# Kernel optimization log

Hardware: AMD Instinct MI355X
Metric: run time of the kernel (lower is better)

The kernel has to match this reference:

```python
import jax, jax.numpy as jnp
import numpy as np

KS = 3                 # kernel_size
DILATIONS = (1, 2, 3)  # dilation list
NUM_HEADS = 6


def _unfold_reflect(x, ks, dil):
    """ReflectionPad2d(dil*(ks-1)//2) + Unfold(ks, dilation=dil).
    x: [B, C, H, W] -> [B, C*ks*ks, H, W] (channel-major like torch Unfold)."""
    pad = dil * (ks - 1) // 2
    xp = jnp.pad(x, ((0, 0), (0, 0), (pad, pad), (pad, pad)), mode='reflect')
    return jax.lax.conv_general_dilated_patches(
        xp, filter_shape=(ks, ks), window_strides=(1, 1), padding='VALID',
        rhs_dilation=(dil, dil))  # [B, C*ks*ks, H, W]


def _dilate_attention(q, k, v, head_dim, ks, dil):
    """q,k,v: [B, c2, H, W] -> [B, H, W, c2]."""
    B, c2, H, W = q.shape
    nh = c2 // head_dim
    scale = head_dim ** (-0.5)
    P = H * W
    k2 = ks * ks
    # q -> [B, nh, P, hd]
    qr = q.reshape(B, nh, head_dim, P).transpose(0, 1, 3, 2)
    # unfold k, v -> [B, c2*k2, H, W], channel order (c, kh, kw)
    ku = _unfold_reflect(k, ks, dil).reshape(B, nh, head_dim, k2, P)
    vu = _unfold_reflect(v, ks, dil).reshape(B, nh, head_dim, k2, P)
    kr = ku.transpose(0, 1, 4, 2, 3)  # [B, nh, P, hd, k2]
    vr = vu.transpose(0, 1, 4, 3, 2)  # [B, nh, P, k2, hd]
    scores = jnp.einsum('bnpd,bnpdk->bnpk', qr, kr) * scale
    attn = jax.nn.softmax(scores, axis=-1)
    out = jnp.einsum('bnpk,bnpkd->bnpd', attn, vr)  # [B, nh, P, hd]
    return out.transpose(0, 2, 1, 3).reshape(B, H, W, nh * head_dim)


def _forward(x, pos_w, pos_b, qkv_w, proj_w):
    B, C, H, W = x.shape
    nd = len(DILATIONS)
    c2 = C // nd
    head_dim = C // NUM_HEADS
    # depthwise 3x3 positional conv (groups=C) + residual
    pe = jax.lax.conv_general_dilated(
        x, pos_w, window_strides=(1, 1), padding=((1, 1), (1, 1)),
        dimension_numbers=('NCHW', 'OIHW', 'NCHW'), feature_group_count=C)
    x = x + pe + pos_b[None, :, None, None]
    # 1x1 qkv conv
    qkv = jnp.einsum('oc,bchw->bohw', qkv_w, x)  # [B, 3C, H, W]
    # 'b (three nd c2) h w -> nd three b c2 h w'
    qkv = qkv.reshape(B, 3, nd, c2, H, W).transpose(2, 1, 0, 3, 4, 5)
    outs = []
    for i, dil in enumerate(DILATIONS):
        o = _dilate_attention(qkv[i, 0], qkv[i, 1], qkv[i, 2], head_dim, KS, dil)
        outs.append(o.transpose(0, 3, 1, 2))  # [B, c2, H, W]
    xo = jnp.concatenate(outs, axis=1)  # [B, C, H, W], dilation-major channels
    return jnp.einsum('oc,bchw->bohw', proj_w, xo)


def setup_inputs() -> dict:
    key = jax.random.key(0)
    ks = jax.random.split(key, 5)
    B, C, H, W = 4, 192, 128, 128
    return {
        'x': jax.random.normal(ks[0], (B, C, H, W), dtype=jnp.float32),
        'pos_w': jax.random.normal(ks[1], (C, 1, 3, 3), dtype=jnp.float32) * 0.05,
        'pos_b': jax.random.normal(ks[2], (C,), dtype=jnp.float32) * 0.05,
        'qkv_w': jax.random.normal(ks[3], (3 * C, C), dtype=jnp.float32) * (C ** -0.5),
        'proj_w': jax.random.normal(ks[4], (C, C), dtype=jnp.float32) * (C ** -0.5),
    }


def reference(x, pos_w, pos_b, qkv_w, proj_w):
    return _forward(x, pos_w, pos_b, qkv_w, proj_w)
```

## Files before the change

### kernel.cpp

```cpp
#include <hip/hip_runtime.h>
#include <hip/hip_bf16.h>
#include <math.h>

#define Hdim 128
#define Wdim 128
#define HW   16384
#define Cdim 192
#define Bdim 4
#define QKVC 576
#define NTOT (Bdim * HW)

typedef __attribute__((ext_vector_type(8))) short short8;
typedef __attribute__((ext_vector_type(4))) short short4v;
typedef __attribute__((ext_vector_type(4))) float f32x4;

__device__ __forceinline__ void async_ld16(void* lds, const void* g) {
    __builtin_amdgcn_global_load_lds(
        (const __attribute__((address_space(1))) void*)g,
        (__attribute__((address_space(3))) void*)lds, 16, 0, 0);
}
__device__ __forceinline__ float lo16(unsigned u) { return __uint_as_float(u << 16); }
__device__ __forceinline__ float hi16(unsigned u) { return __uint_as_float(u & 0xffff0000u); }

__global__ void convert_w(const float* __restrict__ qkv_w,
                          const float* __restrict__ proj_w,
                          __hip_bfloat16* __restrict__ Wq,
                          __hip_bfloat16* __restrict__ Wp) {
    int i = blockIdx.x * 256 + threadIdx.x;
    if (i < QKVC * Cdim) {
        Wq[i] = __float2bfloat16(qkv_w[i]);
    } else {
        int j = i - QKVC * Cdim;
        Wp[j] = __float2bfloat16(proj_w[j]);
    }
}

__global__ __launch_bounds__(256, 4)
void posconv_nhwc(const float* __restrict__ x,
                  const float* __restrict__ pos_w,
                  const float* __restrict__ pos_b,
                  __hip_bfloat16* __restrict__ Xb) {
    __shared__ __hip_bfloat16 tile[Cdim][68];
    __shared__ float wts[Cdim * 9];
    __shared__ float bs[Cdim];
    int t = threadIdx.x;
    for (int i = t; i < Cdim * 9; i += 256) wts[i] = pos_w[i];
    if (t < Cdim) bs[t] = pos_b[t];
    __syncthreads();

    int id = blockIdx.x;
    int xj = id & 7;
    int r  = id >> 3;
    int b  = r >> 5;
    int k  = r & 31;
    int h  = xj * 16 + (k >> 1);
    int wbase = (k & 1) * 64;
    int p0 = (b << 14) + h * Wdim + wbase;
    const float* xim = x + (size_t)b * Cdim * HW;

#pragma unroll
    for (int it = 0; it < 12; ++it) {
        int quad = t & 15;
        int c = it * 16 + (t >> 4);
        int w0 = wbase + quad * 4;
        const float* xc = xim + (size_t)c * HW;
        const float* wt = wts + c * 9;
        float o0, o1, o2, o3;
        {
            const float* xr = xc + h * Wdim;
            float4 f = *(const float4*)(xr + w0);
            float L = (w0 > 0) ? xr[w0 - 1] : 0.f;
            float R = (w0 + 4 < Wdim) ? xr[w0 + 4] : 0.f;
            float b0 = bs[c];
            float w_0 = wt[3], w_1 = wt[4], w_2 = wt[5];
            o0 = f.x + b0 + w_0 * L   + w_1 * f.x + w_2 * f.y;
            o1 = f.y + b0 + w_0 * f.x + w_1 * f.y + w_2 * f.z;
            o2 = f.z + b0 + w_0 * f.y + w_1 * f.z + w_2 * f.w;
            o3 = f.w + b0 + w_0 * f.z + w_1 * f.w + w_2 * R;
        }
        if (h > 0) {
            const float* xr = xc + (h - 1) * Wdim;
            float4 f = *(const float4*)(xr + w0);
            float L = (w0 > 0) ? xr[w0 - 1] : 0.f;
            float R = (w0 + 4 < Wdim) ? xr[w0 + 4] : 0.f;
            float w_0 = wt[0], w_1 = wt[1], w_2 = wt[2];
            o0 += w_0 * L   + w_1 * f.x + w_2 * f.y;
            o1 += w_0 * f.x + w_1 * f.y + w_2 * f.z;
            o2 += w_0 * f.y + w_1 * f.z + w_2 * f.w;
            o3 += w_0 * f.z + w_1 * f.w + w_2 * R;
        }
        if (h < Hdim - 1) {
            const float* xr = xc + (h + 1) * Wdim;
            float4 f = *(const float4*)(xr + w0);
            float L = (w0 > 0) ? xr[w0 - 1] : 0.f;
            float R = (w0 + 4 < Wdim) ? xr[w0 + 4] : 0.f;
            float w_0 = wt[6], w_1 = wt[7], w_2 = wt[8];
            o0 += w_0 * L   + w_1 * f.x + w_2 * f.y;
            o1 += w_0 * f.x + w_1 * f.y + w_2 * f.z;
            o2 += w_0 * f.y + w_1 * f.z + w_2 * f.w;
            o3 += w_0 * f.z + w_1 * f.w + w_2 * R;
        }
        short4v pk;
        __hip_bfloat16 bv;
        bv = __float2bfloat16(o0); pk[0] = *(short*)&bv;
        bv = __float2bfloat16(o1); pk[1] = *(short*)&bv;
        bv = __float2bfloat16(o2); pk[2] = *(short*)&bv;
        bv = __float2bfloat16(o3); pk[3] = *(short*)&bv;
        *(short4v*)(void*)&tile[c][quad * 4] = pk;
    }
    __syncthreads();

#pragma unroll
    for (int it = 0; it < 6; ++it) {
        int pl = t & 63;
        int cgq = it * 4 + (t >> 6);
        union { unsigned short u[8]; short8 v; } o;
#pragma unroll
        for (int j = 0; j < 8; ++j)
            o.u[j] = *(const unsigned short*)&tile[cgq * 8 + j][pl];
        *(short8*)(void*)(Xb + (size_t)(p0 + pl) * Cdim + cgq * 8) = o.v;
    }
}

template <int MODE, int MT>
__global__ __launch_bounds__(256, 2)
void gemm_mfma(const __hip_bfloat16* __restrict__ Wb,
               const __hip_bfloat16* __restrict__ Xt,
               void* __restrict__ Cout) {
    __shared__ __hip_bfloat16 As[64 * 32];
    __shared__ __hip_bfloat16 Bs[256 * 32];
    const int t = threadIdx.x;
    const int w = t >> 6, l = t & 63;
    const int lq = l >> 4, lr = l & 15;
    const int id = blockIdx.x;
    const int xj = id & 7;
    const int rest = id >> 3;
    const int m0 = (rest % MT) * 64;
    const int n0 = ((rest / MT) * 8 + xj) * 256;

    f32x4 acc[4][4] = {};

    for (int kt = 0; kt < 6; ++kt) {
        const int k0 = kt * 32;
        {
            int m = t >> 2, kc = t & 3;
            async_ld16(As + t * 8, Wb + (size_t)(m0 + m) * Cdim + k0 + kc * 8);
        }
#pragma unroll
        for (int it = 0; it < 4; ++it) {
            int idx = it * 256 + t;
            int n = idx >> 2, kc = idx & 3;
            const __hip_bfloat16* src;
            if (MODE == 0)
                src = Xt + (size_t)(n0 + n) * Cdim + k0 + kc * 8;
            else
                src = Xt + (size_t)kt * ((size_t)NTOT * 32) +
                      (size_t)(n0 + n) * 32 + kc * 8;
            async_ld16(Bs + idx * 8, src);
        }
        __syncthreads();

        short8 af[4], bf[4];
#pragma unroll
        for (int i = 0; i < 4; ++i)
            af[i] = *(const short8*)(void*)(As + (i * 16 + lr) * 32 + lq * 8);
#pragma unroll
        for (int j = 0; j < 4; ++j)
            bf[j] = *(const short8*)(void*)(Bs + (w * 64 + j * 16 + lr) * 32 + lq * 8);
#pragma unroll
        for (int i = 0; i < 4; ++i)
#pragma unroll
            for (int j = 0; j < 4; ++j)
                acc[i][j] = __builtin_amdgcn_mfma_f32_16x16x32_bf16(
                    af[i], bf[j], acc[i][j], 0, 0, 0);
        __syncthreads();
    }

#pragma unroll
    for (int i = 0; i < 4; ++i) {
        int mb = m0 + i * 16 + lq * 4;
#pragma unroll
        for (int j = 0; j < 4; ++j) {
            int n = n0 + w * 64 + j * 16 + lr;
            if (MODE == 0) {
                int three = mb / 192, rem = mb % 192;
                int pi = rem >> 6, pn = (rem >> 5) & 1, d4 = rem & 31;
                size_t plane = (size_t)((three * 3 + pi) * 2 + pn);
                __hip_bfloat16* dst = (__hip_bfloat16*)Cout +
                    plane * ((size_t)NTOT * 32) + (size_t)n * 32 + d4;
                short4v pk;
#pragma unroll
                for (int r = 0; r < 4; ++r) {
                    __hip_bfloat16 bv = __float2bfloat16(acc[i][j][r]);
                    pk[r] = *(short*)&bv;
                }
                *(short4v*)(void*)dst = pk;
            } else {
                int b = n >> 14, p = n & (HW - 1);
#pragma unroll
                for (int r = 0; r < 4; ++r)
                    ((float*)Cout)[((size_t)(b * Cdim + mb + r)) * HW + p] =
                        acc[i][j][r];
            }
        }
    }
}

__global__ __launch_bounds__(256, 3)
void attn_kernel(const __hip_bfloat16* __restrict__ QKV,
                 __hip_bfloat16* __restrict__ AO) {
    __shared__ __align__(16) unsigned char lds[6][8192];

    int t = threadIdx.x;
    int pix = t >> 1, s = t & 1;
    int id = blockIdx.x;
    int xj = id & 7;
    int rest = id >> 3;
    int cb = rest >> 4;
    int k16 = rest & 15;
    int h = xj * 16 + k16;
    int b = cb / 6, comb = cb % 6;
    int dil = (comb >> 1) + 1;

    int w = pix;
    int col = (b << 14) + h * Wdim + w;

    const size_t PS = (size_t)NTOT * 32;
    const __hip_bfloat16* Qp = QKV + (size_t)comb * PS;
    const __hip_bfloat16* Kp = Qp + 6 * PS;
    const __hip_bfloat16* Vp = Qp + 12 * PS;

    const uint4* qp = (const uint4*)(Qp + (size_t)col * 32) + s * 2;
    uint4 qv0 = qp[0], qv1 = qp[1];

    int hh[3];
#pragma unroll
    for (int kh = 0; kh < 3; ++kh) {
        int v = h + (kh - 1) * dil;
        hh[kh] = v < 0 ? -v : (v >= Hdim ? 2 * Hdim - 2 - v : v);
    }
    int j0 = t, j1 = t + 256;
    int g0 = j0 ^ ((j0 >> 3) & 7);
    int g1 = j1 ^ ((j1 >> 3) & 7);
#pragma unroll
    for (int r = 0; r < 3; ++r) {
        size_t rowe = ((size_t)(b << 14) + (size_t)hh[r] * Wdim) * 32;
        async_ld16(&lds[r][j0 * 16],     Kp + rowe + g0 * 8);
        async_ld16(&lds[r][j1 * 16],     Kp + rowe + g1 * 8);
        async_ld16(&lds[r + 3][j0 * 16], Vp + rowe + g0 * 8);
        async_ld16(&lds[r + 3][j1 * 16], Vp + rowe + g1 * 8);
    }
    __syncthreads();

    float q[16];
    {
        uint4 x = qv0;
        q[0] = lo16(x.x); q[1] = hi16(x.x);
        q[2] = lo16(x.y); q[3] = hi16(x.y);
        q[4] = lo16(x.z); q[5] = hi16(x.z);
        q[6] = lo16(x.w); q[7] = hi16(x.w);
        x = qv1;
        q[8]  = lo16(x.x); q[9]  = hi16(x.x);
        q[10] = lo16(x.y); q[11] = hi16(x.y);
        q[12] = lo16(x.z); q[13] = hi16(x.z);
        q[14] = lo16(x.w); q[15] = hi16(x.w);
    }

    int coff[3];
#pragma unroll
    for (int kw = 0; kw < 3; ++kw) {
        int ww = w + (kw - 1) * dil;
        ww = ww < 0 ? -ww : (ww >= Wdim ? 2 * Wdim - 2 - ww : ww);
        int i0 = 4 * ww + 2 * s;
        coff[kw] = (i0 ^ ((ww >> 1) & 7)) * 16;
    }

    float sc[9];
#pragma unroll
    for (int kh = 0; kh < 3; ++kh)
#pragma unroll
        for (int kw = 0; kw < 3; ++kw) {
            uint4 xa = *(const uint4*)(void*)&lds[kh][coff[kw]];
            uint4 xb = *(const uint4*)(void*)&lds[kh][coff[kw] ^ 16];
            float p0 = 0.f;
            p0 += q[0] * lo16(xa.x) + q[1] * hi16(xa.x);
            p0 += q[2] * lo16(xa.y) + q[3] * hi16(xa.y);
            p0 += q[4] * lo16(xa.z) + q[5] * hi16(xa.z);
            p0 += q[6] * lo16(xa.w) + q[7] * hi16(xa.w);
            p0 += q[8]  * lo16(xb.x) + q[9]  * hi16(xb.x);
            p0 += q[10] * lo16(xb.y) + q[11] * hi16(xb.y);
            p0 += q[12] * lo16(xb.z) + q[13] * hi16(xb.z);
            p0 += q[14] * lo16(xb.w) + q[15] * hi16(xb.w);
            sc[kh * 3 + kw] = p0;
        }

#pragma unroll
    for (int j = 0; j < 9; ++j)
        sc[j] = (sc[j] + __shfl_xor(sc[j], 1, 64)) * 0.17677669529663687f;

    float m = sc[0];
#pragma unroll
    for (int j = 1; j < 9; ++j) m = fmaxf(m, sc[j]);
    float sum = 0.f;
#pragma unroll
    for (int j = 0; j < 9; ++j) { sc[j] = __expf(sc[j] - m); sum += sc[j]; }
    float inv = 1.f / sum;

    float acc[16] = {};
#pragma unroll
    for (int kh = 0; kh < 3; ++kh)
#pragma unroll
        for (int kw = 0; kw < 3; ++kw) {
            float a = sc[kh * 3 + kw];
            uint4 xa = *(const uint4*)(void*)&lds[kh + 3][coff[kw]];
            uint4 xb = *(const uint4*)(void*)&lds[kh + 3][coff[kw] ^ 16];
            acc[0] += a * lo16(xa.x); acc[1] += a * hi16(xa.x);
            acc[2] += a * lo16(xa.y); acc[3] += a * hi16(xa.y);
            acc[4] += a * lo16(xa.z); acc[5] += a * hi16(xa.z);
            acc[6] += a * lo16(xa.w); acc[7] += a * hi16(xa.w);
            acc[8]  += a * lo16(xb.x); acc[9]  += a * hi16(xb.x);
            acc[10] += a * lo16(xb.y); acc[11] += a * hi16(xb.y);
            acc[12] += a * lo16(xb.z); acc[13] += a * hi16(xb.z);
            acc[14] += a * lo16(xb.w); acc[15] += a * hi16(xb.w);
        }

    union { unsigned short hu[16]; short8 v[2]; } o;
#pragma unroll
    for (int d = 0; d < 16; ++d) {
        __hip_bfloat16 bv = __float2bfloat16(acc[d] * inv);
        o.hu[d] = *(unsigned short*)&bv;
    }
    short8* dst = (short8*)(void*)(AO + (size_t)comb * PS + (size_t)col * 32 + s * 16);
#pragma unroll
    for (int u = 0; u < 2; ++u) dst[u] = o.v[u];
}

extern "C" void kernel_launch(void* const* d_in, const int* in_sizes, int n_in,
                              void* d_out, int out_size, void* d_ws, size_t ws_size,
                              hipStream_t stream) {
    const float* x      = (const float*)d_in[0];
    const float* pos_w  = (const float*)d_in[1];
    const float* pos_b  = (const float*)d_in[2];
    const float* qkv_w  = (const float*)d_in[3];
    const float* proj_w = (const float*)d_in[4];
    float* out = (float*)d_out;

    char* ws = (char*)d_ws;
    __hip_bfloat16* Xb  = (__hip_bfloat16*)ws;
    __hip_bfloat16* QKV = (__hip_bfloat16*)(ws + (size_t)25165824);
    __hip_bfloat16* AO  = (__hip_bfloat16*)(ws + (size_t)100663296);
    __hip_bfloat16* Wq  = (__hip_bfloat16*)(ws + (size_t)125829120);
    __hip_bfloat16* Wp  = (__hip_bfloat16*)(ws + (size_t)126050304);

    convert_w<<<(QKVC * Cdim + Cdim * Cdim) / 256, 256, 0, stream>>>(
        qkv_w, proj_w, Wq, Wp);

    posconv_nhwc<<<NTOT / 64, 256, 0, stream>>>(x, pos_w, pos_b, Xb);

    gemm_mfma<0, 9><<<2304, 256, 0, stream>>>(Wq, Xb, QKV);

    attn_kernel<<<3072, 256, 0, stream>>>(QKV, AO);

    gemm_mfma<1, 3><<<768, 256, 0, stream>>>(Wp, AO, out);
}
```

Measured before the change: 203.7 us.

## Restructure positional conv to stage rows in LDS via async loads

The depthwise positional conv is reworked. Each block now handles 16 channels of a full image row and stages the three needed input rows into swizzled LDS with global_load_lds. Horizontal neighbours come from wave shuffles instead of extra scalar global loads, and weights and bias live in registers with masks handling the vertical edges. This is meant to cut redundant global reads and uncoalesced edge loads. In exchange it launches a larger grid with narrower 16-channel output writes per pixel, and a redundant first compute loop is left in the code.

Result: faster. 187.4 us (-8.0%).

```diff
diff --git a/kernel.cpp b/kernel.cpp
--- a/kernel.cpp
+++ b/kernel.cpp
@@ -35,91 +35,154 @@
     }
 }
 
-__global__ __launch_bounds__(256, 4)
+__global__ __launch_bounds__(256, 5)
 void posconv_nhwc(const float* __restrict__ x,
                   const float* __restrict__ pos_w,
                   const float* __restrict__ pos_b,
                   __hip_bfloat16* __restrict__ Xb) {
-    __shared__ __hip_bfloat16 tile[Cdim][68];
-    __shared__ float wts[Cdim * 9];
-    __shared__ float bs[Cdim];
+    __shared__ __align__(16) float xs[3 * 16 * 128];
+    __shared__ __hip_bfloat16 tile[16][132];
+
     int t = threadIdx.x;
-    for (int i = t; i < Cdim * 9; i += 256) wts[i] = pos_w[i];
-    if (t < Cdim) bs[t] = pos_b[t];
-    __syncthreads();
-
     int id = blockIdx.x;
     int xj = id & 7;
-    int r  = id >> 3;
-    int b  = r >> 5;
-    int k  = r & 31;
-    int h  = xj * 16 + (k >> 1);
-    int wbase = (k & 1) * 64;
-    int p0 = (b << 14) + h * Wdim + wbase;
-    const float* xim = x + (size_t)b * Cdim * HW;
-
-#pragma unroll
-    for (int it = 0; it < 12; ++it) {
-        int quad = t & 15;
-        int c = it * 16 + (t >> 4);
-        int w0 = wbase + quad * 4;
-        const float* xc = xim + (size_t)c * HW;
-        const float* wt = wts + c * 9;
-        float o0, o1, o2, o3;
-        {
-            const float* xr = xc + h * Wdim;
-            float4 f = *(const float4*)(xr + w0);
-            float L = (w0 > 0) ? xr[w0 - 1] : 0.f;
-            float R = (w0 + 4 < Wdim) ? xr[w0 + 4] : 0.f;
-            float b0 = bs[c];
-            float w_0 = wt[3], w_1 = wt[4], w_2 = wt[5];
-            o0 = f.x + b0 + w_0 * L   + w_1 * f.x + w_2 * f.y;
-            o1 = f.y + b0 + w_0 * f.x + w_1 * f.y + w_2 * f.z;
-            o2 = f.z + b0 + w_0 * f.y + w_1 * f.z + w_2 * f.w;
-            o3 = f.w + b0 + w_0 * f.z + w_1 * f.w + w_2 * R;
-        }
-        if (h > 0) {
-            const float* xr = xc + (h - 1) * Wdim;
-            float4 f = *(const float4*)(xr + w0);
-            float L = (w0 > 0) ? xr[w0 - 1] : 0.f;
-            float R = (w0 + 4 < Wdim) ? xr[w0 + 4] : 0.f;
-            float w_0 = wt[0], w_1 = wt[1], w_2 = wt[2];
-            o0 += w_0 * L   + w_1 * f.x + w_2 * f.y;
-            o1 += w_0 * f.x + w_1 * f.y + w_2 * f.z;
-            o2 += w_0 * f.y + w_1 * f.z + w_2 * f.w;
-            o3 += w_0 * f.z + w_1 * f.w + w_2 * R;
-        }
-        if (h < Hdim - 1) {
-            const float* xr = xc + (h + 1) * Wdim;
-            float4 f = *(const float4*)(xr + w0);
-            float L = (w0 > 0) ? xr[w0 - 1] : 0.f;
-            float R = (w0 + 4 < Wdim) ? xr[w0 + 4] : 0.f;
-            float w_0 = wt[6], w_1 = wt[7], w_2 = wt[8];
-            o0 += w_0 * L   + w_1 * f.x + w_2 * f.y;
-            o1 += w_0 * f.x + w_1 * f.y + w_2 * f.z;
-            o2 += w_0 * f.y + w_1 * f.z + w_2 * f.w;
-            o3 += w_0 * f.z + w_1 * f.w + w_2 * R;
-        }
-        short4v pk;
-        __hip_bfloat16 bv;
-        bv = __float2bfloat16(o0); pk[0] = *(short*)&bv;
-        bv = __float2bfloat16(o1); pk[1] = *(short*)&bv;
-        bv = __float2bfloat16(o2); pk[2] = *(short*)&bv;
-        bv = __float2bfloat16(o3); pk[3] = *(short*)&bv;
-        *(short4v*)(void*)&tile[c][quad * 4] = pk;
+    int r_ = id >> 3;
+    int rb = r_ & 15;
+    int cg = (r_ >> 4) % 12;
+    int b  = (r_ >> 4) / 12;
+    int h  = xj * 16 + rb;
+
+    int hm = h > 0 ? h - 1 : 0;
+    int hp = h < Hdim - 1 ? h + 1 : Hdim - 1;
+    int hh0 = hm, hh1 = h, hh2 = hp;
+
+    int ch = t >> 4;
+    int qh = t & 15;
+    int cglob = cg * 16 + ch;
+
+    const float* wp = pos_w + cglob * 9;
+    float w0 = wp[0], w1 = wp[1], w2 = wp[2];
+    float w3 = wp[3], w4 = wp[4], w5 = wp[5];
+    float w6 = wp[6], w7 = wp[7], w8 = wp[8];
+    float bias = pos_b[cglob];
+    float m0 = (h > 0) ? 1.f : 0.f;
+    float m2 = (h < Hdim - 1) ? 1.f : 0.f;
+    w0 *= m0; w1 *= m0; w2 *= m0;
+    w6 *= m2; w7 *= m2; w8 *= m2;
+
+    {
+        const float* xg = x + (size_t)(b * Cdim + cg * 16) * HW;
+#pragma unroll
+        for (int k = 0; k < 6; ++k) {
+            int u = t + k * 256;
+            int rowi = u >> 5;
+            int ql = u & 31;
+            int rr = rowi >> 4;
+            int sch = rowi & 15;
+            int hr = rr == 0 ? hh0 : (rr == 1 ? hh1 : hh2);
+            int qs = ql ^ sch;
+            async_ld16((char*)xs + (size_t)u * 16,
+                       xg + (size_t)sch * HW + hr * Wdim + qs * 4);
+        }
     }
     __syncthreads();
 
-#pragma unroll
-    for (int it = 0; it < 6; ++it) {
-        int pl = t & 63;
-        int cgq = it * 4 + (t >> 6);
-        union { unsigned short u[8]; short8 v; } o;
-#pragma unroll
-        for (int j = 0; j < 8; ++j)
-            o.u[j] = *(const unsigned short*)&tile[cgq * 8 + j][pl];
-        *(short8*)(void*)(Xb + (size_t)(p0 + pl) * Cdim + cgq * 8) = o.v;
-    }
+    float out[8];
+    const char* xsb = (const char*)xs;
+#pragma unroll
+    for (int rr = 0; rr < 3; ++rr) {
+        const char* rowb = xsb + (size_t)(rr * 16 + ch) * 512;
+        float4 lo = *(const float4*)(rowb + (((2 * qh)     ^ ch) * 16));
+        float4 hi = *(const float4*)(rowb + (((2 * qh + 1) ^ ch) * 16));
+        float L = __shfl_up(hi.w, 1, 64);
+        float R = __shfl_down(lo.x, 1, 64);
+        if (qh == 0)  L = 0.f;
+        if (qh == 15) R = 0.f;
+        float v0 = L,    v1 = lo.x, v2 = lo.y, v3 = lo.z, v4 = lo.w;
+        float v5 = hi.x, v6 = hi.y, v7 = hi.z, v8 = hi.w, v9 = R;
+        float wa, wb, wc;
+        if (rr == 0)      { wa = w0; wb = w1; wc = w2; }
+        else if (rr == 1) { wa = w3; wb = w4; wc = w5; }
+        else              { wa = w6; wb = w7; wc = w8; }
+        if (rr == 1) {
+            out[0] = v1 + bias; out[1] = v2 + bias; out[2] = v3 + bias;
+            out[3] = v4 + bias; out[4] = v5 + bias; out[5] = v6 + bias;
+            out[6] = v7 + bias; out[7] = v8 + bias;
+        }
+        if (rr == 0) {
+            out[0] = wa * v0 + wb * v1 + wc * v2;
+            out[1] = wa * v1 + wb * v2 + wc * v3;
+            out[2] = wa * v2 + wb * v3 + wc * v4;
+            out[3] = wa * v3 + wb * v4 + wc * v5;
+            out[4] = wa * v4 + wb * v5 + wc * v6;
+            out[5] = wa * v5 + wb * v6 + wc * v7;
+            out[6] = wa * v6 + wb * v7 + wc * v8;
+            out[7] = wa * v7 + wb * v8 + wc * v9;
+        } else if (rr == 1) {
+            out[0] += wa * v0 + wb * v1 + wc * v2;
+            out[1] += wa * v1 + wb * v2 + wc * v3;
+            out[2] += wa * v2 + wb * v3 + wc * v4;
+            out[3] += wa * v3 + wb * v4 + wc * v5;
+            out[4] += wa * v4 + wb * v5 + wc * v6;
+            out[5] += wa * v5 + wb * v6 + wc * v7;
+            out[6] += wa * v6 + wb * v7 + wc * v8;
+            out[7] += wa * v7 + wb * v8 + wc * v9;
+        } else {
+            out[0] += wa * v0 + wb * v1 + wc * v2;
+            out[1] += wa * v1 + wb * v2 + wc * v3;
+            out[2] += wa * v2 + wb * v3 + wc * v4;
+            out[3] += wa * v3 + wb * v4 + wc * v5;
+            out[4] += wa * v4 + wb * v5 + wc * v6;
+            out[5] += wa * v5 + wb * v6 + wc * v7;
+            out[6] += wa * v6 + wb * v7 + wc * v8;
+            out[7] += wa * v7 + wb * v8 + wc * v9;
+        }
+    }
+
+
+    {
+        const char* r0b = xsb + (size_t)(0 * 16 + ch) * 512;
+        const char* r1b = xsb + (size_t)(1 * 16 + ch) * 512;
+        const char* r2b = xsb + (size_t)(2 * 16 + ch) * 512;
+        float4 lo0 = *(const float4*)(r0b + (((2 * qh)     ^ ch) * 16));
+        float4 hi0 = *(const float4*)(r0b + (((2 * qh + 1) ^ ch) * 16));
+        float4 lo1 = *(const float4*)(r1b + (((2 * qh)     ^ ch) * 16));
+        float4 hi1 = *(const float4*)(r1b + (((2 * qh + 1) ^ ch) * 16));
+        float4 lo2 = *(const float4*)(r2b + (((2 * qh)     ^ ch) * 16));
+        float4 hi2 = *(const float4*)(r2b + (((2 * qh + 1) ^ ch) * 16));
+        float L0 = __shfl_up(hi0.w, 1, 64), R0 = __shfl_down(lo0.x, 1, 64);
+        float L1 = __shfl_up(hi1.w, 1, 64), R1 = __shfl_down(lo1.x, 1, 64);
+        float L2 = __shfl_up(hi2.w, 1, 64), R2 = __shfl_down(lo2.x, 1, 64);
+        if (qh == 0)  { L0 = 0.f; L1 = 0.f; L2 = 0.f; }
+        if (qh == 15) { R0 = 0.f; R1 = 0.f; R2 = 0.f; }
+        float a0[10] = {L0, lo0.x, lo0.y, lo0.z, lo0.w, hi0.x, hi0.y, hi0.z, hi0.w, R0};
+        float a1[10] = {L1, lo1.x, lo1.y, lo1.z, lo1.w, hi1.x, hi1.y, hi1.z, hi1.w, R1};
+        float a2[10] = {L2, lo2.x, lo2.y, lo2.z, lo2.w, hi2.x, hi2.y, hi2.z, hi2.w, R2};
+#pragma unroll
+        for (int i = 0; i < 8; ++i) {
+            out[i] = a1[i + 1] + bias
+                   + w0 * a0[i] + w1 * a0[i + 1] + w2 * a0[i + 2]
+                   + w3 * a1[i] + w4 * a1[i + 1] + w5 * a1[i + 2]
+                   + w6 * a2[i] + w7 * a2[i + 1] + w8 * a2[i + 2];
+        }
+    }
+
+    union { unsigned short u[8]; short8 v; } pk;
+#pragma unroll
+    for (int i = 0; i < 8; ++i) {
+        __hip_bfloat16 bv = __float2bfloat16(out[i]);
+        pk.u[i] = *(unsigned short*)&bv;
+    }
+    *(short8*)(void*)&tile[ch][qh * 8] = pk.v;
+    __syncthreads();
+
+    int px = t >> 1, s2 = t & 1;
+    union { unsigned short u[8]; short8 v; } o;
+#pragma unroll
+    for (int j = 0; j < 8; ++j)
+        o.u[j] = *(const unsigned short*)&tile[s2 * 8 + j][px];
+    size_t p0img = (size_t)(b << 14) + (size_t)h * Wdim;
+    *(short8*)(void*)(Xb + (p0img + px) * Cdim + cg * 16 + s2 * 8) = o.v;
 }
 
 template <int MODE, int MT>
@@ -355,7 +418,7 @@
     convert_w<<<(QKVC * Cdim + Cdim * Cdim) / 256, 256, 0, stream>>>(
         qkv_w, proj_w, Wq, Wp);
 
-    posconv_nhwc<<<NTOT / 64, 256, 0, stream>>>(x, pos_w, pos_b, Xb);
+    posconv_nhwc<<<6144, 256, 0, stream>>>(x, pos_w, pos_b, Xb);
 
     gemm_mfma<0, 9><<<2304, 256, 0, stream>>>(Wq, Xb, QKV);
 
```
